# Kernel tuning notes

Hardware: AMD Instinct MI355X
Metric: run time of the kernel (lower is better)

Reference implementation:

```python
import jax, jax.numpy as jnp
import numpy as np

H = 16  # num heads
EPS = 1e-5


def layer_norm(x, g, b):
    mu = jnp.mean(x, axis=-1, keepdims=True)
    var = jnp.var(x, axis=-1, keepdims=True)
    return (x - mu) * jax.lax.rsqrt(var + EPS) * g + b


def setup_inputs() -> dict:
    key = jax.random.key(0)
    ks = jax.random.split(key, 8)
    B, T, D, TE = 4, 4096, 1024, 1024
    s = 0.02  # weight init scale
    return {
        "x": jax.random.normal(ks[0], (B, T, D), jnp.float32),
        "emb": jax.random.normal(ks[1], (B, 1, TE), jnp.float32),
        "gate_msa": jax.random.normal(ks[2], (B, 1, D), jnp.float32),
        "norm_g": jnp.ones((D,), jnp.float32),
        "norm_b": jnp.zeros((D,), jnp.float32),
        "Wq": jax.random.normal(ks[3], (D, D), jnp.float32) * s,
        "bq": jnp.zeros((D,), jnp.float32),
        "Wk": jax.random.normal(ks[4], (D, D), jnp.float32) * s,
        "bk": jnp.zeros((D,), jnp.float32),
        "Wv": jax.random.normal(ks[5], (D, D), jnp.float32) * s,
        "bv": jnp.zeros((D,), jnp.float32),
        "emb_W": jax.random.normal(ks[6], (TE, 2 * D), jnp.float32) * s,
        "emb_b": jnp.zeros((2 * D,), jnp.float32),
        "sn_g": jnp.ones((D,), jnp.float32),
        "sn_b": jnp.zeros((D,), jnp.float32),
        "out_W": jax.random.normal(ks[7], (D, D), jnp.float32) * s,
        "out_b": jnp.zeros((D,), jnp.float32),
    }


def reference(x, emb, gate_msa, norm_g, norm_b, Wq, bq, Wk, bk, Wv, bv,
              emb_W, emb_b, sn_g, sn_b, out_W, out_b):
    B, T, D = x.shape
    dh = D // H
    xn = layer_norm(x, norm_g, norm_b)
    q = (xn @ Wq + bq).reshape(B, T, H, dh)
    k = (xn @ Wk + bk).reshape(B, T, H, dh)
    v = (xn @ Wv + bv).reshape(B, T, H, dh)
    q = jax.nn.softmax(q, axis=-1)      # feature-dim softmax
    k = jax.nn.softmax(k, axis=1)       # temporal softmax
    ctx = jnp.einsum('bnhd,bnhl->bhdl', k, v)  # [B,H,dh,dh] context
    y = jnp.einsum('bnhd,bhdl->bnhl', q, ctx).reshape(B, T, D)
    # StylizationBlock (dropout=0 eval semantics)
    emb_out = jax.nn.silu(emb) @ emb_W + emb_b        # [B,1,2D]
    scale, shift = jnp.split(emb_out, 2, axis=-1)
    h = layer_norm(y, sn_g, sn_b) * (1.0 + scale) + shift
    h = jax.nn.silu(h) @ out_W + out_b
    return x + gate_msa * h
```

## Files before the change

### kernel.cpp

```cpp
#include <hip/hip_runtime.h>
#include <stdint.h>

typedef unsigned short u16;
typedef float f32x4 __attribute__((ext_vector_type(4)));
typedef __bf16 bf16x8 __attribute__((ext_vector_type(8)));

__device__ __forceinline__ float b2f(u16 u) {
    union { unsigned int i; float f; } w; w.i = ((unsigned int)u) << 16; return w.f;
}
__device__ __forceinline__ u16 f2b(float f) {
    union { float f; unsigned int i; } w; w.f = f;
    unsigned int r = w.i + 0x7fffu + ((w.i >> 16) & 1u);
    return (u16)(r >> 16);
}
__device__ __forceinline__ void gload16(const void* g, void* l) {
    __builtin_amdgcn_global_load_lds(
        (const __attribute__((address_space(1))) unsigned int*)g,
        (__attribute__((address_space(3))) unsigned int*)l, 16, 0, 0);
}

__global__ __launch_bounds__(256) void prep_k(
    const float* __restrict__ Wq, const float* __restrict__ Wk, const float* __restrict__ Wv,
    const float* __restrict__ Wo, const float* __restrict__ bq, const float* __restrict__ bk,
    const float* __restrict__ bv, const float* __restrict__ ob,
    u16* __restrict__ WqkvT, u16* __restrict__ WoT, float* __restrict__ biasAll,
    float* __restrict__ zeroBase)
{
    int bz = blockIdx.x, tid = threadIdx.x;
    if (bz < 4096) {
        int z = bz >> 10, rem = bz & 1023;
        const float* src = (z == 0) ? Wq : (z == 1) ? Wk : (z == 2) ? Wv : Wo;
        u16* dst = (z < 3) ? (WqkvT + (size_t)z * 1024 * 1024) : WoT;
        __shared__ u16 tile[32][33];
        int tx = tid & 31, ty = tid >> 5;
        int n0 = (rem & 31) * 32, k0 = (rem >> 5) * 32;
#pragma unroll
        for (int i = 0; i < 4; i++) tile[ty + 8 * i][tx] = f2b(src[(size_t)(k0 + ty + 8 * i) * 1024 + n0 + tx]);
        __syncthreads();
#pragma unroll
        for (int i = 0; i < 4; i++) dst[(size_t)(n0 + ty + 8 * i) * 1024 + k0 + tx] = tile[tx][ty + 8 * i];
    } else if (bz < 4112) {
        int i = (bz - 4096) * 256 + tid;
        float v;
        if (i < 1024) v = bq[i];
        else if (i < 2048) v = bk[i - 1024];
        else if (i < 3072) v = bv[i - 2048];
        else v = ob[i - 3072];
        biasAll[i] = v;
    } else {
        int e = (bz - 4112) * 256 + tid;
        ((float4*)zeroBase)[e] = make_float4(0.f, 0.f, 0.f, 0.f);
    }
}

__global__ __launch_bounds__(256) void ln_x(
    const float* __restrict__ x, const float* __restrict__ g, const float* __restrict__ bt,
    u16* __restrict__ xn)
{
    int row = blockIdx.x, tid = threadIdx.x;
    const float* xr = x + (size_t)row * 1024;
    float4 u = *(const float4*)(xr + tid * 4);
    float v0 = u.x, v1 = u.y, v2 = u.z, v3 = u.w;
    float s = v0 + v1 + v2 + v3;
    float s2 = v0 * v0 + v1 * v1 + v2 * v2 + v3 * v3;
#pragma unroll
    for (int m = 32; m > 0; m >>= 1) { s += __shfl_xor(s, m, 64); s2 += __shfl_xor(s2, m, 64); }
    __shared__ float red[8];
    int w = tid >> 6, lane = tid & 63;
    if (lane == 0) { red[w] = s; red[4 + w] = s2; }
    __syncthreads();
    s = red[0] + red[1] + red[2] + red[3];
    s2 = red[4] + red[5] + red[6] + red[7];
    float mean = s * (1.f / 1024.f);
    float var = s2 * (1.f / 1024.f) - mean * mean;
    float rstd = rsqrtf(var + 1e-5f);
    int c = tid * 4;
    float4 gg = *(const float4*)(g + c);
    float4 bb = *(const float4*)(bt + c);
    ushort4 o;
    o.x = f2b((v0 - mean) * rstd * gg.x + bb.x);
    o.y = f2b((v1 - mean) * rstd * gg.y + bb.y);
    o.z = f2b((v2 - mean) * rstd * gg.z + bb.z);
    o.w = f2b((v3 - mean) * rstd * gg.w + bb.w);
    *(ushort4*)(xn + (size_t)row * 1024 + c) = o;
}

__global__ __launch_bounds__(512, 2) void gemm256(
    const u16* __restrict__ A, const u16* __restrict__ Bt, const float* __restrict__ bias,
    int mode, u16* __restrict__ Qb, u16* __restrict__ Kb, u16* __restrict__ Vb,
    float* __restrict__ colsum, float* __restrict__ Cf,
    const float* __restrict__ Xf, const float* __restrict__ gate)
{
    const int K = 1024;
    __shared__ __align__(16) u16 L[2][2][256 * 64];
    int tid = threadIdx.x, lane = tid & 63, w = tid >> 6;
    int wm = w >> 2, wn = w & 3;
    int NB = gridDim.x;
    int lid = blockIdx.y * NB + blockIdx.x;
    int xcd = lid & 7;
    int i_ = lid >> 3;
    int rowLocal = i_ & 7;
    int colIdx = i_ >> 3;
    size_t rowbase = (size_t)(xcd * 8 + rowLocal) * 256;
    size_t colbase = (size_t)colIdx * 256;
    const u16* Ab = A + rowbase * K;
    const u16* Bb = Bt + colbase * K;
    f32x4 acc[8][4] = {};
    int quad = lane >> 4, mr = lane & 15, swK = mr & 7;
    int srow = lane >> 3;
    int scol = ((lane & 7) ^ srow) * 8;
    u16* A0 = L[0][0]; u16* B0 = L[0][1]; u16* A1 = L[1][0]; u16* B1 = L[1][1];

#define STAGE(ldsmat, gbase, hf, k0) do { \
    _Pragma("unroll") \
    for (int r_ = 0; r_ < 2; r_++) { \
        int rb_ = (hf) * 128 + r_ * 64 + w * 8; \
        gload16((gbase) + (size_t)(rb_ + srow) * 1024 + (k0) + scol, (ldsmat) + rb_ * 64); \
    } } while (0)

#define LDA(dst, src, mh) do { \
    _Pragma("unroll") \
    for (int i2_ = 0; i2_ < 4; i2_++) \
    _Pragma("unroll") \
    for (int kq_ = 0; kq_ < 2; kq_++) \
        dst[i2_ * 2 + kq_] = *(const bf16x8*)&(src)[(wm * 128 + (mh) * 64 + i2_ * 16 + mr) * 64 + (((kq_ * 4 + quad) ^ swK) * 8)]; \
    } while (0)

#define LDB(dst, src, nh) do { \
    _Pragma("unroll") \
    for (int j_ = 0; j_ < 2; j_++) \
    _Pragma("unroll") \
    for (int kq_ = 0; kq_ < 2; kq_++) \
        dst[j_ * 2 + kq_] = *(const bf16x8*)&(src)[(wn * 64 + (nh) * 32 + j_ * 16 + mr) * 64 + (((kq_ * 4 + quad) ^ swK) * 8)]; \
    } while (0)

#define MM(mh, nh, av, bv) do { \
    __builtin_amdgcn_s_setprio(1); \
    _Pragma("unroll") \
    for (int i2_ = 0; i2_ < 4; i2_++) \
    _Pragma("unroll") \
    for (int j_ = 0; j_ < 2; j_++) \
    _Pragma("unroll") \
    for (int kq_ = 0; kq_ < 2; kq_++) \
        acc[(mh) * 4 + i2_][(nh) * 2 + j_] = __builtin_amdgcn_mfma_f32_16x16x32_bf16( \
            av[i2_ * 2 + kq_], bv[j_ * 2 + kq_], acc[(mh) * 4 + i2_][(nh) * 2 + j_], 0, 0, 0); \
    __builtin_amdgcn_s_setprio(0); } while (0)

#define BAR() asm volatile("s_barrier" ::: "memory")
#define VMW(n) asm volatile("s_waitcnt vmcnt(" #n ")" ::: "memory")

    STAGE(A0, Ab, 0, 0); STAGE(A0, Ab, 1, 0);
    STAGE(B0, Bb, 0, 0); STAGE(B0, Bb, 1, 0);
    STAGE(B1, Bb, 0, 64); STAGE(B1, Bb, 1, 64);
    VMW(4);
    BAR();

    bf16x8 a[8], bn0[4], bn1[4];
    for (int t = 0; t < 8; ++t) {
        int k0 = t * 128;
        bool last = (t == 7);
        LDA(a, A0, 0); LDB(bn0, B0, 0);
        STAGE(A1, Ab, 0, k0 + 64);
        BAR(); MM(0, 0, a, bn0); BAR();
        LDB(bn1, B0, 1);
        STAGE(A1, Ab, 1, k0 + 64);
        BAR(); MM(0, 1, a, bn1); BAR();
        LDA(a, A0, 1);
        if (!last) STAGE(B0, Bb, 0, k0 + 128);
        BAR(); MM(1, 1, a, bn1); BAR();
        if (!last) STAGE(B0, Bb, 1, k0 + 128);
        BAR(); MM(1, 0, a, bn0);
        if (last) { VMW(0); } else { VMW(4); }
        BAR();
        LDA(a, A1, 0); LDB(bn0, B1, 0);
        if (!last) STAGE(A0, Ab, 0, k0 + 128);
        BAR(); MM(0, 0, a, bn0); BAR();
        LDB(bn1, B1, 1);
        if (!last) STAGE(A0, Ab, 1, k0 + 128);
        BAR(); MM(0, 1, a, bn1); BAR();
        LDA(a, A1, 1);
        if (!last) STAGE(B1, Bb, 0, k0 + 192);
        BAR(); MM(1, 1, a, bn1); BAR();
        if (!last) STAGE(B1, Bb, 1, k0 + 192);
        BAR(); MM(1, 0, a, bn0);
        if (!last) VMW(4);
        BAR();
    }
#undef STAGE
#undef LDA
#undef LDB
#undef MM
#undef BAR
#undef VMW

    int colj[4]; float bj[4];
#pragma unroll
    for (int j = 0; j < 4; j++) { colj[j] = (int)colbase + wn * 64 + j * 16 + mr; bj[j] = bias[colj[j]]; }
    int creg = (int)colbase + wn * 64;
    if (mode == 0) {
        u16* Ct = (u16*)L;
        if (creg < 1024) {
#pragma unroll
            for (int i = 0; i < 8; i++) {
#pragma unroll
                for (int r = 0; r < 4; r++) {
                    int lr = wm * 128 + i * 16 + quad * 4 + r;
                    float v[4], m = -1e30f, ss = 0.f;
#pragma unroll
                    for (int j = 0; j < 4; j++) { v[j] = acc[i][j][r] + bj[j]; m = fmaxf(m, v[j]); }
#pragma unroll
                    for (int s = 1; s < 16; s <<= 1) m = fmaxf(m, __shfl_xor(m, s, 64));
#pragma unroll
                    for (int j = 0; j < 4; j++) { v[j] = __expf(v[j] - m); ss += v[j]; }
#pragma unroll
                    for (int s = 1; s < 16; s <<= 1) ss += __shfl_xor(ss, s, 64);
                    float inv = 1.f / ss;
#pragma unroll
                    for (int j = 0; j < 4; j++)
                        Ct[lr * 256 + wn * 64 + ((j ^ quad) * 16) + mr] = f2b(v[j] * inv);
                }
            }
        } else if (creg < 2048) {
            int b_ = (int)(rowbase >> 12);
            float csum[4] = {};
#pragma unroll
            for (int i = 0; i < 8; i++) {
#pragma unroll
                for (int r = 0; r < 4; r++) {
                    int lr = wm * 128 + i * 16 + quad * 4 + r;
#pragma unroll
                    for (int j = 0; j < 4; j++) {
                        float e = __expf(acc[i][j][r] + bj[j]);
                        Ct[lr * 256 + wn * 64 + ((j ^ quad) * 16) + mr] = f2b(e);
                        csum[j] += e;
                    }
                }
            }
#pragma unroll
            for (int j = 0; j < 4; j++) {
                csum[j] += __shfl_xor(csum[j], 16, 64);
                csum[j] += __shfl_xor(csum[j], 32, 64);
                if (quad == 0) atomicAdd(&colsum[b_ * 1024 + (colj[j] - 1024)], csum[j]);
            }
        } else {
#pragma unroll
            for (int i = 0; i < 8; i++) {
#pragma unroll
                for (int r = 0; r < 4; r++) {
                    int lr = wm * 128 + i * 16 + quad * 4 + r;
#pragma unroll
                    for (int j = 0; j < 4; j++)
                        Ct[lr * 256 + wn * 64 + ((j ^ quad) * 16) + mr] = f2b(acc[i][j][r] + bj[j]);
                }
            }
        }
        __syncthreads();
        u16* dst = (colIdx < 4) ? Qb : (colIdx < 8) ? Kb : Vb;
        int dcol0 = (int)colbase & 1023;
#pragma unroll
        for (int k = 0; k < 16; ++k) {
            int e = k * 512 + tid;
            int row = e >> 5, pos = e & 31;
            int posl = pos ^ (((row >> 2) & 3) << 1);
            *(uint4*)&dst[(rowbase + row) * 1024 + dcol0 + pos * 8] =
                *(const uint4*)&Ct[row * 256 + posl * 8];
        }
        return;
    }
    {
        float* Cs32 = (float*)L;
        int b_ = (int)(rowbase >> 12);
        int q1 = quad & 1;
#pragma unroll 1
        for (int pass = 0; pass < 2; ++pass) {
            if (wm == pass) {
#pragma unroll
                for (int i = 0; i < 8; i++) {
#pragma unroll
                    for (int r = 0; r < 4; r++) {
                        int lr = i * 16 + quad * 4 + r;
#pragma unroll
                        for (int j = 0; j < 4; j++)
                            Cs32[lr * 256 + wn * 64 + ((j ^ q1) * 16) + mr] = acc[i][j][r] + bj[j];
                    }
                }
            }
            __syncthreads();
#pragma unroll
            for (int k = 0; k < 16; ++k) {
                int e = k * 512 + tid;
                int row = e >> 6, pos = e & 63;
                int posl = pos ^ (((row >> 2) & 1) << 2);
                size_t grow = rowbase + pass * 128 + row;
                int col = (int)colbase + pos * 4;
                float4 c4 = *(const float4*)&Cs32[row * 256 + posl * 4];
                float4 xf = *(const float4*)&Xf[grow * 1024 + col];
                float4 g4 = *(const float4*)&gate[b_ * 1024 + col];
                float4 o;
                o.x = xf.x + g4.x * c4.x;
                o.y = xf.y + g4.y * c4.y;
                o.z = xf.z + g4.z * c4.z;
                o.w = xf.w + g4.w * c4.w;
                *(float4*)&Cf[grow * 1024 + col] = o;
            }
            __syncthreads();
        }
    }
}

__global__ __launch_bounds__(256) void ctx_k(
    const u16* __restrict__ kbuf, const u16* __restrict__ vbuf,
    const float* __restrict__ colsum, float* __restrict__ ctx)
{
    int ch = blockIdx.x, h = blockIdx.y, b = blockIdx.z;
    __shared__ __align__(16) float Es[16][64];
    __shared__ __align__(16) float Vs[16][64];
    int tid = threadIdx.x;
    int td = tid >> 4, tl = tid & 15;
    int lr = tid >> 4, lc = (tid & 15) * 4;
    const float* cs = colsum + b * 1024 + h * 64 + lc;
    float4 inv4 = make_float4(1.f / cs[0], 1.f / cs[1], 1.f / cs[2], 1.f / cs[3]);
    float acc[4][4] = {};
    size_t rowbase = (size_t)b * 4096 + ch * 512;
    for (int g = 0; g < 32; ++g) {
        size_t base = (rowbase + g * 16 + lr) * 1024 + h * 64 + lc;
        ushort4 kv = *(const ushort4*)&kbuf[base];
        ushort4 vv = *(const ushort4*)&vbuf[base];
        *(float4*)&Es[lr][lc] = make_float4(b2f(kv.x) * inv4.x, b2f(kv.y) * inv4.y,
                                            b2f(kv.z) * inv4.z, b2f(kv.w) * inv4.w);
        *(float4*)&Vs[lr][lc] = make_float4(b2f(vv.x), b2f(vv.y), b2f(vv.z), b2f(vv.w));
        __syncthreads();
#pragma unroll
        for (int n = 0; n < 16; n++) {
            f32x4 e4 = *(const f32x4*)&Es[n][td * 4];
            f32x4 v4 = *(const f32x4*)&Vs[n][tl * 4];
#pragma unroll
            for (int i = 0; i < 4; i++)
#pragma unroll
                for (int j = 0; j < 4; j++) acc[i][j] += e4[i] * v4[j];
        }
        __syncthreads();
    }
    float* cb = ctx + (size_t)(b * 16 + h) * 4096;
#pragma unroll
    for (int i = 0; i < 4; i++)
#pragma unroll
        for (int j = 0; j < 4; j++)
            atomicAdd(&cb[(td * 4 + i) * 64 + tl * 4 + j], acc[i][j]);
}

__global__ __launch_bounds__(256) void embout_k(
    const float* __restrict__ emb, const float* __restrict__ embW, float* __restrict__ eo)
{
    int cb = blockIdx.x, kc = blockIdx.y;
    __shared__ float semb[128];
    int tid = threadIdx.x;
    if (tid < 128) {
        int b = tid >> 5, kk = tid & 31;
        float xv = emb[b * 1024 + kc * 32 + kk];
        semb[tid] = xv / (1.f + __expf(-xv));
    }
    __syncthreads();
    int o = cb * 256 + tid;
    float a0 = 0, a1 = 0, a2 = 0, a3 = 0;
    for (int kk = 0; kk < 32; kk++) {
        float wv = embW[(size_t)(kc * 32 + kk) * 2048 + o];
        a0 += semb[kk] * wv; a1 += semb[32 + kk] * wv;
        a2 += semb[64 + kk] * wv; a3 += semb[96 + kk] * wv;
    }
    atomicAdd(&eo[o], a0);
    atomicAdd(&eo[2048 + o], a1);
    atomicAdd(&eo[4096 + o], a2);
    atomicAdd(&eo[6144 + o], a3);
}

__global__ __launch_bounds__(256) void y_k(
    const u16* __restrict__ q, const float* __restrict__ ctx, u16* __restrict__ y)
{
    int mc = blockIdx.x, h = blockIdx.y, b = blockIdx.z;
    __shared__ __align__(16) u16 Qs[128 * 64];
    __shared__ __align__(16) u16 Cs[64 * 72];
    int tid = threadIdx.x, lane = tid & 63, w = tid >> 6;
    size_t row0 = (size_t)b * 4096 + (size_t)mc * 128;
    const u16* Qb = q + row0 * 1024 + h * 64;
    int sr = tid >> 3, g_ = tid & 7;
    int scb = (g_ ^ (sr & 7)) * 8;
#pragma unroll
    for (int p = 0; p < 4; p++) {
        int r = p * 32 + sr;
        *(uint4*)&Qs[r * 64 + scb] = *(const uint4*)&Qb[(size_t)r * 1024 + g_ * 8];
    }
    const float* Cb = ctx + (size_t)(b * 16 + h) * 4096;
#pragma unroll
    for (int rep = 0; rep < 16; ++rep) {
        int e = tid + rep * 256;
        int d = e >> 6, l = e & 63;
        Cs[l * 72 + d] = f2b(Cb[e]);
    }
    __syncthreads();
    int quad = lane >> 4, mr = lane & 15;
    int swA = mr & 7;
    f32x4 acc[2][4] = {};
#pragma unroll
    for (int kk = 0; kk < 64; kk += 32) {
        bf16x8 a[2], bb[4];
#pragma unroll
        for (int i = 0; i < 2; i++)
            a[i] = *(const bf16x8*)&Qs[(w * 32 + i * 16 + mr) * 64 + ((((kk >> 3) + quad) ^ swA) * 8)];
#pragma unroll
        for (int j = 0; j < 4; j++) bb[j] = *(const bf16x8*)&Cs[(j * 16 + mr) * 72 + kk + quad * 8];
#pragma unroll
        for (int i = 0; i < 2; i++)
#pragma unroll
            for (int j = 0; j < 4; j++)
                acc[i][j] = __builtin_amdgcn_mfma_f32_16x16x32_bf16(a[i], bb[j], acc[i][j], 0, 0, 0);
    }
#pragma unroll
    for (int i = 0; i < 2; i++)
#pragma unroll
        for (int j = 0; j < 4; j++)
#pragma unroll
            for (int r = 0; r < 4; r++) {
                size_t row = row0 + w * 32 + i * 16 + quad * 4 + r;
                int col = h * 64 + j * 16 + mr;
                y[row * 1024 + col] = f2b(acc[i][j][r]);
            }
}

__global__ __launch_bounds__(256) void style_k(
    u16* __restrict__ y, const float* __restrict__ eo, const float* __restrict__ embb,
    const float* __restrict__ sng, const float* __restrict__ snb)
{
    int row = blockIdx.x, tid = threadIdx.x, b = row >> 12;
    u16* yr = y + (size_t)row * 1024;
    ushort4 u = *(const ushort4*)(yr + tid * 4);
    float vv[4] = { b2f(u.x), b2f(u.y), b2f(u.z), b2f(u.w) };
    float s = vv[0] + vv[1] + vv[2] + vv[3];
    float s2 = vv[0] * vv[0] + vv[1] * vv[1] + vv[2] * vv[2] + vv[3] * vv[3];
#pragma unroll
    for (int m = 32; m > 0; m >>= 1) { s += __shfl_xor(s, m, 64); s2 += __shfl_xor(s2, m, 64); }
    __shared__ float red[8];
    int w = tid >> 6, lane = tid & 63;
    if (lane == 0) { red[w] = s; red[4 + w] = s2; }
    __syncthreads();
    s = red[0] + red[1] + red[2] + red[3];
    s2 = red[4] + red[5] + red[6] + red[7];
    float mean = s * (1.f / 1024.f);
    float var = s2 * (1.f / 1024.f) - mean * mean;
    float rstd = rsqrtf(var + 1e-5f);
    int c = tid * 4;
    ushort4 o;
    u16* op = (u16*)&o;
#pragma unroll
    for (int i = 0; i < 4; i++) {
        int cc = c + i;
        float scale = eo[b * 2048 + cc] + embb[cc];
        float shift = eo[b * 2048 + 1024 + cc] + embb[1024 + cc];
        float hn = (vv[i] - mean) * rstd * sng[cc] + snb[cc];
        float hh = hn * (1.f + scale) + shift;
        op[i] = f2b(hh / (1.f + __expf(-hh)));
    }
    *(ushort4*)(yr + c) = o;
}

extern "C" void kernel_launch(void* const* d_in, const int* in_sizes, int n_in,
                              void* d_out, int out_size, void* d_ws, size_t ws_size,
                              hipStream_t stream)
{
    const float* x    = (const float*)d_in[0];
    const float* emb  = (const float*)d_in[1];
    const float* gate = (const float*)d_in[2];
    const float* ng   = (const float*)d_in[3];
    const float* nb   = (const float*)d_in[4];
    const float* Wq   = (const float*)d_in[5];
    const float* bq   = (const float*)d_in[6];
    const float* Wk   = (const float*)d_in[7];
    const float* bk   = (const float*)d_in[8];
    const float* Wv   = (const float*)d_in[9];
    const float* bv   = (const float*)d_in[10];
    const float* embW = (const float*)d_in[11];
    const float* embB = (const float*)d_in[12];
    const float* sng  = (const float*)d_in[13];
    const float* snb  = (const float*)d_in[14];
    const float* Wo   = (const float*)d_in[15];
    const float* ob   = (const float*)d_in[16];
    float* out = (float*)d_out;

    uint8_t* ws = (uint8_t*)d_ws;
    size_t off = 0;
    auto alloc = [&](size_t bytes) { void* p = ws + off; off += (bytes + 255) & ~(size_t)255; return p; };
    u16*   WqkvT   = (u16*)alloc(3072ull * 1024 * 2);
    u16*   WoT     = (u16*)alloc(1024ull * 1024 * 2);
    float* biasAll = (float*)alloc(4096 * 4);
    float* colsum  = (float*)alloc(4096 * 4);
    float* ctx     = (float*)alloc(64ull * 64 * 64 * 4);
    float* embout  = (float*)alloc(4ull * 2048 * 4);
    u16*   XN      = (u16*)alloc(16384ull * 1024 * 2);
    u16*   BUF0    = (u16*)alloc(16384ull * 1024 * 2);
    u16*   BUF1    = (u16*)alloc(16384ull * 1024 * 2);
    u16*   BUF2    = (u16*)alloc(16384ull * 1024 * 2);

    prep_k<<<4380, 256, 0, stream>>>(Wq, Wk, Wv, Wo, bq, bk, bv, ob, WqkvT, WoT, biasAll, colsum);
    ln_x<<<16384, 256, 0, stream>>>(x, ng, nb, XN);
    gemm256<<<dim3(12, 64), 512, 0, stream>>>(XN, WqkvT, biasAll, 0,
                                              BUF0, BUF1, BUF2, colsum, nullptr, nullptr, nullptr);
    ctx_k<<<dim3(8, 16, 4), 256, 0, stream>>>(BUF1, BUF2, colsum, ctx);
    embout_k<<<dim3(8, 32), 256, 0, stream>>>(emb, embW, embout);
    y_k<<<dim3(32, 16, 4), 256, 0, stream>>>(BUF0, ctx, XN);
    style_k<<<16384, 256, 0, stream>>>(XN, embout, embB, sng, snb);
    gemm256<<<dim3(4, 64), 512, 0, stream>>>(XN, WoT, biasAll + 3072, 2,
                                             nullptr, nullptr, nullptr, nullptr, out, x, gate);
}
```

Before: 424.2 us.

## Restructure GEMM K-loop into double-buffered tile pipeline with fewer barriers

Replaces the hand-unrolled K-loop, which used eight barrier-separated MFMA quarters per 128-K step, with a TILE macro that stages the next 64-K A and B tiles into the alternate buffer while computing the current one. Each tile now uses four barriers, drains all outstanding loads (vmcnt 0) at the end, and preloads the next tile's first fragments before the barrier. The aim is less barrier overhead and better overlap of global-to-LDS loads with MFMA work. The risk is that waiting on every load each tile exposes memory latency, and the non-unrolled loop can add scheduling overhead.

Measured after the change: 416.7 us. About the same (-1.8%).

```diff
diff --git a/kernel.cpp b/kernel.cpp
--- a/kernel.cpp
+++ b/kernel.cpp
@@ -151,41 +151,41 @@
 
     STAGE(A0, Ab, 0, 0); STAGE(A0, Ab, 1, 0);
     STAGE(B0, Bb, 0, 0); STAGE(B0, Bb, 1, 0);
-    STAGE(B1, Bb, 0, 64); STAGE(B1, Bb, 1, 64);
-    VMW(4);
+    VMW(0);
     BAR();
 
     bf16x8 a[8], bn0[4], bn1[4];
-    for (int t = 0; t < 8; ++t) {
-        int k0 = t * 128;
-        bool last = (t == 7);
-        LDA(a, A0, 0); LDB(bn0, B0, 0);
-        STAGE(A1, Ab, 0, k0 + 64);
-        BAR(); MM(0, 0, a, bn0); BAR();
-        LDB(bn1, B0, 1);
-        STAGE(A1, Ab, 1, k0 + 64);
-        BAR(); MM(0, 1, a, bn1); BAR();
-        LDA(a, A0, 1);
-        if (!last) STAGE(B0, Bb, 0, k0 + 128);
-        BAR(); MM(1, 1, a, bn1); BAR();
-        if (!last) STAGE(B0, Bb, 1, k0 + 128);
-        BAR(); MM(1, 0, a, bn0);
-        if (last) { VMW(0); } else { VMW(4); }
-        BAR();
-        LDA(a, A1, 0); LDB(bn0, B1, 0);
-        if (!last) STAGE(A0, Ab, 0, k0 + 128);
-        BAR(); MM(0, 0, a, bn0); BAR();
-        LDB(bn1, B1, 1);
-        if (!last) STAGE(A0, Ab, 1, k0 + 128);
-        BAR(); MM(0, 1, a, bn1); BAR();
-        LDA(a, A1, 1);
-        if (!last) STAGE(B1, Bb, 0, k0 + 192);
-        BAR(); MM(1, 1, a, bn1); BAR();
-        if (!last) STAGE(B1, Bb, 1, k0 + 192);
-        BAR(); MM(1, 0, a, bn0);
-        if (!last) VMW(4);
-        BAR();
-    }
+    LDA(a, A0, 0); LDB(bn0, B0, 0);
+
+#define TILE(T, cA, cB, nA, nB) do { \
+    const int kN_ = ((T) + 1) * 64; \
+     \
+    if ((T) < 15) { STAGE(nA, Ab, 0, kN_); STAGE(nA, Ab, 1, kN_); } \
+    LDB(bn1, cB, 1); \
+    MM(0, 0, a, bn0); \
+    BAR(); \
+     \
+    if ((T) < 15) { STAGE(nB, Bb, 0, kN_); STAGE(nB, Bb, 1, kN_); } \
+    MM(0, 1, a, bn1); \
+    BAR(); \
+     \
+    LDA(a, cA, 1); \
+    MM(1, 0, a, bn0); \
+    BAR(); \
+     \
+    MM(1, 1, a, bn1); \
+    VMW(0); \
+    if ((T) < 15) { LDA(a, nA, 0); LDB(bn0, nB, 0); } \
+    BAR(); \
+    } while (0)
+
+#pragma unroll 1
+    for (int t2 = 0; t2 < 8; ++t2) {
+        int T = 2 * t2;
+        TILE(T, A0, B0, A1, B1);
+        TILE((T + 1), A1, B1, A0, B0);
+    }
+#undef TILE
 #undef STAGE
 #undef LDA
 #undef LDB
```
